# Optimization experiments

Hardware: AMD Instinct MI355X
Metric: run time of the kernel (lower is better)

Reference implementation:

```python
import jax, jax.numpy as jnp
import numpy as np

RATIO = 1.25   # res_s / res_r (1.0mm slices on 0.8mm volume grid)
N_ITER = 10


def _psf_offsets(psf):
    # psf [Kz,Ky,Kx]; offsets returned in (x,y,z) order, volume-voxel units,
    # centered integer grid (applied in the slice frame before rotation).
    Kz, Ky, Kx = psf.shape
    zs = jnp.arange(Kz, dtype=psf.dtype) - (Kz - 1) / 2.0
    ys = jnp.arange(Ky, dtype=psf.dtype) - (Ky - 1) / 2.0
    xs = jnp.arange(Kx, dtype=psf.dtype) - (Kx - 1) / 2.0
    gz, gy, gx = jnp.meshgrid(zs, ys, xs, indexing='ij')
    offs = jnp.stack([gx, gy, gz], -1).reshape(-1, 3)  # [K,3]
    return offs, psf.reshape(-1)


def _base_grid(Hs, Ws, dtype):
    # slice pixel coords, centered, scaled to volume-voxel units; (x,y,z=0)
    ys = (jnp.arange(Hs, dtype=dtype) - (Hs - 1) / 2.0) * RATIO
    xs = (jnp.arange(Ws, dtype=dtype) - (Ws - 1) / 2.0) * RATIO
    gy, gx = jnp.meshgrid(ys, xs, indexing='ij')
    return jnp.stack([gx, gy, jnp.zeros_like(gx)], -1)  # [Hs,Ws,3]


def _corners(pts, D, H, W):
    x, y, z = pts[..., 0], pts[..., 1], pts[..., 2]
    x0 = jnp.floor(x); y0 = jnp.floor(y); z0 = jnp.floor(z)
    fx, fy, fz = x - x0, y - y0, z - z0
    return (x0.astype(jnp.int32), y0.astype(jnp.int32), z0.astype(jnp.int32), fx, fy, fz)


def _trilerp_gather(vol, pts):
    # vol [D,H,W]; pts [...,3] in (x,y,z) volume-voxel coords; zero outside.
    D, H, W = vol.shape
    x0, y0, z0, fx, fy, fz = _corners(pts, D, H, W)
    out = jnp.zeros(pts.shape[:-1], vol.dtype)
    for dz in (0, 1):
        zi = z0 + dz; wz = fz if dz else (1.0 - fz); vz = (zi >= 0) & (zi < D)
        for dy in (0, 1):
            yi = y0 + dy; wy = fy if dy else (1.0 - fy); vy = vz & (yi >= 0) & (yi < H)
            for dx in (0, 1):
                xi = x0 + dx; wx = fx if dx else (1.0 - fx)
                valid = vy & (xi >= 0) & (xi < W)
                v = vol[jnp.clip(zi, 0, D - 1), jnp.clip(yi, 0, H - 1), jnp.clip(xi, 0, W - 1)]
                out = out + jnp.where(valid, wz * wy * wx * v, 0.0)
    return out


def _splat_add(vol, pts, vals):
    # adjoint of _trilerp_gather: scatter-add vals into vol at pts
    D, H, W = vol.shape
    x0, y0, z0, fx, fy, fz = _corners(pts, D, H, W)
    for dz in (0, 1):
        zi = z0 + dz; wz = fz if dz else (1.0 - fz); vz = (zi >= 0) & (zi < D)
        for dy in (0, 1):
            yi = y0 + dy; wy = fy if dy else (1.0 - fy); vy = vz & (yi >= 0) & (yi < H)
            for dx in (0, 1):
                xi = x0 + dx; wx = fx if dx else (1.0 - fx)
                valid = vy & (xi >= 0) & (xi < W)
                contrib = jnp.where(valid, wz * wy * wx * vals, 0.0)
                vol = vol.at[jnp.clip(zi, 0, D - 1), jnp.clip(yi, 0, H - 1), jnp.clip(xi, 0, W - 1)].add(contrib)
    return vol


def _points(base, off, R, t, center):
    pts = base + off                                             # [Hs,Ws,3] slice frame
    return jnp.einsum('nij,hwj->nhwi', R, pts) + t[:, None, None, :] + center  # [N,Hs,Ws,3]


def A_op(vol, transforms, psf, slice_shape):
    # slice acquisition: PSF-blurred trilinear sampling of vol along each slice
    D, H, W = vol.shape
    R, t = transforms[:, :, :3], transforms[:, :, 3]
    center = jnp.array([(W - 1) / 2.0, (H - 1) / 2.0, (D - 1) / 2.0], vol.dtype)
    base = _base_grid(slice_shape[0], slice_shape[1], vol.dtype)
    offs, w = _psf_offsets(psf)
    N = transforms.shape[0]

    def step(acc, ow):
        off, wk = ow
        ptv = _points(base, off, R, t, center)
        return acc + wk * _trilerp_gather(vol, ptv), None

    out, _ = jax.lax.scan(step, jnp.zeros((N,) + tuple(slice_shape), vol.dtype), (offs, w))
    return out


def At_op(slices, transforms, psf, vol_shape):
    # adjoint: splat PSF-weighted slice values back into the volume
    D, H, W = vol_shape
    R, t = transforms[:, :, :3], transforms[:, :, 3]
    center = jnp.array([(W - 1) / 2.0, (H - 1) / 2.0, (D - 1) / 2.0], slices.dtype)
    base = _base_grid(slices.shape[1], slices.shape[2], slices.dtype)
    offs, w = _psf_offsets(psf)

    def step(acc, ow):
        off, wk = ow
        ptv = _points(base, off, R, t, center)
        return _splat_add(acc, ptv, wk * slices), None

    out, _ = jax.lax.scan(step, jnp.zeros(vol_shape, slices.dtype), (offs, w))
    return out


def _srr_cg(vol, slices, transforms, psf):
    v = vol[0, 0]            # [D,H,W]
    y = slices[:, 0]         # [N,Hs,Ws]
    vol_shape = v.shape
    slice_shape = y.shape[1:]
    AtA = lambda x: At_op(A_op(x, transforms, psf, slice_shape), transforms, psf, vol_shape)
    b = At_op(y, transforms, psf, vol_shape)
    # CG with x0 = volume image (average_init=False), tol=0, mu=0, p=z=None
    x = v
    r = b - AtA(x)
    p = r
    rr = jnp.vdot(r, r)
    for i in range(N_ITER):
        Ap = AtA(p)
        alpha = rr / jnp.vdot(p, Ap)
        x = x + alpha * p
        if i == N_ITER - 1:
            break
        r = r - alpha * Ap
        rr_new = jnp.vdot(r, r)
        p = r + (rr_new / rr) * p
        rr = rr_new
    return jax.nn.relu(x)    # output_relu=True


def setup_inputs() -> dict:
    key = jax.random.key(0)
    k1, k2 = jax.random.split(key)
    D = H = W = 128
    N, Hs, Ws = 48, 128, 128
    vol = jax.random.uniform(k1, (1, 1, D, H, W), jnp.float32)
    slices = jax.random.uniform(k2, (N, 1, Hs, Ws), jnp.float32)
    # rigid slice->volume transforms: small random rotations, slices stacked along z
    rng = np.random.default_rng(0)
    trans = np.zeros((N, 3, 4), np.float32)
    spacing = 2.0 / 0.8  # thickness / res_r = 2.5 voxels
    for n in range(N):
        ax, ay, az = rng.uniform(-0.15, 0.15, 3)
        Rx = np.array([[1, 0, 0], [0, np.cos(ax), -np.sin(ax)], [0, np.sin(ax), np.cos(ax)]])
        Ry = np.array([[np.cos(ay), 0, np.sin(ay)], [0, 1, 0], [-np.sin(ay), 0, np.cos(ay)]])
        Rz = np.array([[np.cos(az), -np.sin(az), 0], [np.sin(az), np.cos(az), 0], [0, 0, 1]])
        trans[n, :, :3] = Rz @ Ry @ Rx
        trans[n, :, 3] = rng.uniform(-3.0, 3.0, 3)
        trans[n, 2, 3] += (n - (N - 1) / 2.0) * spacing
    # Gaussian PSF from resolution ratios: sigma_xy = 1.2*RATIO/2.3548, sigma_z = 2.5/2.3548
    def gauss(k, s):
        r = np.arange(k) - (k - 1) / 2.0
        return np.exp(-0.5 * (r / s) ** 2)
    psf = gauss(5, 2.5 / 2.3548)[:, None, None] * gauss(3, 1.2 * RATIO / 2.3548)[None, :, None] \
          * gauss(3, 1.2 * RATIO / 2.3548)[None, None, :]
    psf = (psf / psf.sum()).astype(np.float32)
    return {"vol": vol, "slices": slices, "transforms": jnp.asarray(trans), "psf": jnp.asarray(psf)}


def reference(vol, slices, transforms, psf):
    return _srr_cg(vol, slices, transforms, psf)
```

## Files before the change

kernel.cpp:

```cpp
#include <hip/hip_runtime.h>

#define NVOX (128*128*128)
#define NK 45
#define NSL 48
#define LDSF 9800

__device__ __forceinline__ float trilerp_gather_g(const float* __restrict__ v,
                                                  float x, float y, float z)
{
    float x0f = floorf(x), y0f = floorf(y), z0f = floorf(z);
    int x0 = (int)x0f, y0 = (int)y0f, z0 = (int)z0f;
    float fx = x - x0f, fy = y - y0f, fz = z - z0f;

    if (((unsigned)x0 < 127u) & ((unsigned)y0 < 127u) & ((unsigned)z0 < 127u)) {
        const float* p = v + z0*16384 + y0*128 + x0;
        float v000 = p[0],     v001 = p[1];
        float v010 = p[128],   v011 = p[129];
        float v100 = p[16384], v101 = p[16385];
        float v110 = p[16512], v111 = p[16513];
        float c00 = v000 + fx*(v001 - v000);
        float c01 = v010 + fx*(v011 - v010);
        float c10 = v100 + fx*(v101 - v100);
        float c11 = v110 + fx*(v111 - v110);
        float c0  = c00 + fy*(c01 - c00);
        float c1  = c10 + fy*(c11 - c10);
        return c0 + fz*(c1 - c0);
    }
    if (x0 < -1 || x0 > 127 || y0 < -1 || y0 > 127 || z0 < -1 || z0 > 127)
        return 0.f;
    float acc = 0.f;
#pragma unroll
    for (int dz = 0; dz < 2; ++dz) {
        int zi = z0 + dz;
        if ((unsigned)zi >= 128u) continue;
        float wz = dz ? fz : 1.f - fz;
#pragma unroll
        for (int dy = 0; dy < 2; ++dy) {
            int yi = y0 + dy;
            if ((unsigned)yi >= 128u) continue;
            float wy = dy ? fy : 1.f - fy;
#pragma unroll
            for (int dx = 0; dx < 2; ++dx) {
                int xi = x0 + dx;
                if ((unsigned)xi >= 128u) continue;
                float wx = dx ? fx : 1.f - fx;
                acc += wz*wy*wx * v[zi*16384 + yi*128 + xi];
            }
        }
    }
    return acc;
}

__device__ __forceinline__ void trilerp_splat_g(float* __restrict__ v,
                                                float x, float y, float z, float val)
{
    float x0f = floorf(x), y0f = floorf(y), z0f = floorf(z);
    int x0 = (int)x0f, y0 = (int)y0f, z0 = (int)z0f;
    float fx = x - x0f, fy = y - y0f, fz = z - z0f;
    if (x0 < -1 || x0 > 127 || y0 < -1 || y0 > 127 || z0 < -1 || z0 > 127)
        return;
#pragma unroll
    for (int dz = 0; dz < 2; ++dz) {
        int zi = z0 + dz;
        if ((unsigned)zi >= 128u) continue;
        float wz = dz ? fz : 1.f - fz;
#pragma unroll
        for (int dy = 0; dy < 2; ++dy) {
            int yi = y0 + dy;
            if ((unsigned)yi >= 128u) continue;
            float wy = dy ? fy : 1.f - fy;
#pragma unroll
            for (int dx = 0; dx < 2; ++dx) {
                int xi = x0 + dx;
                if ((unsigned)xi >= 128u) continue;
                float wx = dx ? fx : 1.f - fx;
                unsafeAtomicAdd(v + zi*16384 + yi*128 + xi, val*wz*wy*wx);
            }
        }
    }
}

__global__ void k_shifts(const float* __restrict__ trans, float* __restrict__ shifts)
{
    int i = blockIdx.x * blockDim.x + threadIdx.x;
    if (i >= NSL * NK) return;
    int n = i / NK, k = i % NK;
    int kz = k / 9, ky = (k % 9) / 3, kx = k % 3;
    float ox = (float)(kx - 1);
    float oy = (float)(ky - 1);
    float oz = (float)(kz - 2);
    const float* T = trans + n * 12;
    shifts[i*3+0] = T[0]*ox + T[1]*oy + T[2]*oz  + T[3]  + 63.5f;
    shifts[i*3+1] = T[4]*ox + T[5]*oy + T[6]*oz  + T[7]  + 63.5f;
    shifts[i*3+2] = T[8]*ox + T[9]*oy + T[10]*oz + T[11] + 63.5f;
}

__device__ __forceinline__ void block_reduce_add(double s, double* out)
{
    for (int o = 32; o > 0; o >>= 1) s += __shfl_down(s, o);
    __shared__ double ls[4];
    int lane = threadIdx.x & 63, wid = threadIdx.x >> 6;
    if (lane == 0) ls[wid] = s;
    __syncthreads();
    if (threadIdx.x == 0) atomicAdd(out, ls[0] + ls[1] + ls[2] + ls[3]);
}

__global__ __launch_bounds__(256) void k_gather(const float* __restrict__ vol,
                                                const float* __restrict__ shifts,
                                                const float* __restrict__ psf,
                                                const float* __restrict__ trans,
                                                float* __restrict__ val,
                                                float4* __restrict__ ap_zero,
                                                double* __restrict__ pap)
{
    __shared__ float sh[NK*4];
    int bid = blockIdx.x;
    int swz = (bid & 7) * (NSL * 64 / 8) + (bid >> 3);
    int n = swz >> 6, seg = swz & 63, tid = threadIdx.x;

    int zi = bid * 256 + tid;
    if (zi < NVOX/4) ap_zero[zi] = make_float4(0.f, 0.f, 0.f, 0.f);

    for (int i = tid; i < NK*3; i += 256) sh[i] = shifts[n*NK*3 + i];
    if (tid < NK) sh[NK*3+tid] = psf[tid];
    const float* T = trans + n*12;
    float R00=T[0],R01=T[1],R10=T[4],R11=T[5],R20=T[8],R21=T[9];
    __syncthreads();

    int idx = seg*256 + tid;
    int h = idx >> 7, w = idx & 127;
    float bx = ((float)w - 63.5f)*1.25f;
    float by = ((float)h - 63.5f)*1.25f;
    float rbx = R00*bx + R01*by;
    float rby = R10*bx + R11*by;
    float rbz = R20*bx + R21*by;

    float s = 0.f;
#pragma unroll 3
    for (int k = 0; k < NK; ++k)
        s += sh[NK*3+k] * trilerp_gather_g(vol, rbx + sh[k*3], rby + sh[k*3+1],
                                           rbz + sh[k*3+2]);
    val[n*16384 + idx] = s;

    block_reduce_add((double)s * (double)s, pap);
}

__global__ __launch_bounds__(64) void k_splat(const float* __restrict__ val,
                                              float* __restrict__ pout,
                                              const float* __restrict__ shifts,
                                              const float* __restrict__ psf,
                                              const float* __restrict__ trans)
{
    __shared__ float tile[LDSF];
    __shared__ float sh[NK*4];
    int n = blockIdx.x >> 6, t2 = blockIdx.x & 63;
    int th = t2 >> 3, tw = t2 & 7;
    int lane = threadIdx.x;
    int kbeg = blockIdx.y ? 27 : 0;
    int kend = blockIdx.y ? NK : 27;
    int kcnt = kend - kbeg;

    for (int i = lane; i < NK*3; i += 64) sh[i] = shifts[n*NK*3 + i];
    if (lane < NK) sh[NK*3+lane] = psf[lane];
    const float* T = trans + n*12;
    float R00=T[0],R01=T[1],R10=T[4],R11=T[5],R20=T[8],R21=T[9];
    __syncthreads();

    int kl = kbeg + ((lane < kcnt) ? lane : 0);
    float sx0 = sh[kl*3], sy0 = sh[kl*3+1], sz0 = sh[kl*3+2];
    float sxmn=sx0,sxmx=sx0,symn=sy0,symx=sy0,szmn=sz0,szmx=sz0;
    for (int o = 32; o; o >>= 1) {
        sxmn = fminf(sxmn, __shfl_xor(sxmn,o)); sxmx = fmaxf(sxmx, __shfl_xor(sxmx,o));
        symn = fminf(symn, __shfl_xor(symn,o)); symx = fmaxf(symx, __shfl_xor(symx,o));
        szmn = fminf(szmn, __shfl_xor(szmn,o)); szmx = fmaxf(szmx, __shfl_xor(szmx,o));
    }
    float cbx = ((float)(tw*16) + 7.5f - 63.5f)*1.25f;
    float cby = ((float)(th*16) + 7.5f - 63.5f)*1.25f;
    const float hs = 9.375f;
    float cx = R00*cbx + R01*cby, hx = (fabsf(R00)+fabsf(R01))*hs;
    float cy = R10*cbx + R11*cby, hy = (fabsf(R10)+fabsf(R11))*hs;
    float cz = R20*cbx + R21*cby, hz = (fabsf(R20)+fabsf(R21))*hs;
    int x_lo = (int)floorf(cx-hx+sxmn), x_hi = (int)floorf(cx+hx+sxmx)+1;
    int y_lo = (int)floorf(cy-hy+symn), y_hi = (int)floorf(cy+hy+symx)+1;
    int z_lo = (int)floorf(cz-hz+szmn), z_hi = (int)floorf(cz+hz+szmx)+1;
    int dxs  = x_hi - x_lo + 1;
    dxs |= 1;
    int dys  = y_hi - y_lo + 1;
    int dzs  = z_hi - z_lo + 1;
    int dxdy = dxs * dys;
    int total = dxdy * dzs;

    bool safe = (2.5f*(R00 - fabsf(R01)) >= 2.0f) &&
                (2.5f*(R11 - fabsf(R10)) >= 2.0f);

    if (total <= LDSF) {
        for (int c = lane; c < total; c += 64) tile[c] = 0.f;
        __syncthreads();

        float prbx[4], prby[4], prbz[4], pval[4];
#pragma unroll
        for (int p = 0; p < 4; ++p) {
            int w = tw*16 + 2*(lane & 7)  + (p & 1);
            int h = th*16 + 2*(lane >> 3) + (p >> 1);
            float bx = ((float)w - 63.5f)*1.25f;
            float by = ((float)h - 63.5f)*1.25f;
            prbx[p] = R00*bx + R01*by;
            prby[p] = R10*bx + R11*by;
            prbz[p] = R20*bx + R21*by;
            pval[p] = val[n*16384 + (h<<7) + w];
        }

#pragma unroll 1
        for (int k = kbeg; k < kend; ++k) {
            float sx = sh[k*3], sy = sh[k*3+1], sz = sh[k*3+2], wk = sh[NK*3+k];
#pragma unroll
            for (int p = 0; p < 4; ++p) {
                float x = prbx[p] + sx, y = prby[p] + sy, z = prbz[p] + sz;
                float x0f = floorf(x), y0f = floorf(y), z0f = floorf(z);
                int lx = (int)x0f - x_lo, ly = (int)y0f - y_lo, lz = (int)z0f - z_lo;
                float fx = x - x0f, fy = y - y0f, fz = z - z0f;
                float vw = pval[p] * wk;
                float wx1 = fx, wx0 = 1.f - fx;
                float wy1 = fy, wy0 = 1.f - fy;
                float wz1 = fz, wz0 = 1.f - fz;
                float* q = tile + lz*dxdy + ly*dxs + lx;
                if (safe) {
                    q[0]          += vw*wz0*wy0*wx0;
                    q[1]          += vw*wz0*wy0*wx1;
                    q[dxs]        += vw*wz0*wy1*wx0;
                    q[dxs+1]      += vw*wz0*wy1*wx1;
                    q[dxdy]       += vw*wz1*wy0*wx0;
                    q[dxdy+1]     += vw*wz1*wy0*wx1;
                    q[dxdy+dxs]   += vw*wz1*wy1*wx0;
                    q[dxdy+dxs+1] += vw*wz1*wy1*wx1;
                } else {
                    atomicAdd(q,            vw*wz0*wy0*wx0);
                    atomicAdd(q+1,          vw*wz0*wy0*wx1);
                    atomicAdd(q+dxs,        vw*wz0*wy1*wx0);
                    atomicAdd(q+dxs+1,      vw*wz0*wy1*wx1);
                    atomicAdd(q+dxdy,       vw*wz1*wy0*wx0);
                    atomicAdd(q+dxdy+1,     vw*wz1*wy0*wx1);
                    atomicAdd(q+dxdy+dxs,   vw*wz1*wy1*wx0);
                    atomicAdd(q+dxdy+dxs+1, vw*wz1*wy1*wx1);
                }
            }
        }
        __syncthreads();

        for (int c = lane; c < total; c += 64) {
            float v2 = tile[c];
            if (v2 != 0.f) {
                int lz = c / dxdy;
                int rem = c - lz*dxdy;
                int ly = rem / dxs;
                int lx = rem - ly*dxs;
                int gx = x_lo+lx, gy = y_lo+ly, gz = z_lo+lz;
                if (((unsigned)gx < 128u) & ((unsigned)gy < 128u) & ((unsigned)gz < 128u))
                    unsafeAtomicAdd(pout + gz*16384 + gy*128 + gx, v2);
            }
        }
    } else {
        for (int s2 = 0; s2 < 4; ++s2) {
            int px = s2*64 + lane;
            int ty = px >> 4, tx = px & 15;
            int h = th*16 + ty, w = tw*16 + tx;
            float bx = ((float)w - 63.5f)*1.25f;
            float by = ((float)h - 63.5f)*1.25f;
            float rbx = R00*bx + R01*by;
            float rby = R10*bx + R11*by;
            float rbz = R20*bx + R21*by;
            float v = val[n*16384 + (h<<7) + w];
#pragma unroll 1
            for (int k = kbeg; k < kend; ++k)
                trilerp_splat_g(pout, rbx + sh[k*3], rby + sh[k*3+1],
                                rbz + sh[k*3+2], sh[NK*3+k] * v);
        }
    }
}

__global__ __launch_bounds__(256) void k_init(const float* __restrict__ b,
                                              const float* __restrict__ Ax,
                                              float* __restrict__ r,
                                              float* __restrict__ p,
                                              double* rr0)
{
    double s = 0.0;
    for (int i = blockIdx.x * blockDim.x + threadIdx.x; i < NVOX;
         i += gridDim.x * blockDim.x) {
        float rv = b[i] - Ax[i];
        r[i] = rv;
        p[i] = rv;
        s += (double)rv * (double)rv;
    }
    block_reduce_add(s, rr0);
}

__global__ __launch_bounds__(256) void k_update_xr(float* __restrict__ x,
                                                   float* __restrict__ r,
                                                   const float* __restrict__ p,
                                                   const float* __restrict__ Ap,
                                                   const double* rr, const double* pap,
                                                   double* rrn, int do_r)
{
    float alpha = (float)(rr[0] / pap[0]);
    double s = 0.0;
    for (int i = blockIdx.x * blockDim.x + threadIdx.x; i < NVOX;
         i += gridDim.x * blockDim.x) {
        x[i] += alpha * p[i];
        if (do_r) {
            float rn = r[i] - alpha * Ap[i];
            r[i] = rn;
            s += (double)rn * (double)rn;
        }
    }
    block_reduce_add(s, rrn);
}

__global__ __launch_bounds__(256) void k_update_p(float* __restrict__ p,
                                                  const float* __restrict__ r,
                                                  const double* rrn, const double* rro)
{
    float beta = (float)(rrn[0] / rro[0]);
    for (int i = blockIdx.x * blockDim.x + threadIdx.x; i < NVOX;
         i += gridDim.x * blockDim.x)
        p[i] = r[i] + beta * p[i];
}

__global__ __launch_bounds__(256) void k_relu(const float* __restrict__ x,
                                              float* __restrict__ out)
{
    for (int i = blockIdx.x * blockDim.x + threadIdx.x; i < NVOX;
         i += gridDim.x * blockDim.x)
        out[i] = fmaxf(x[i], 0.f);
}

extern "C" void kernel_launch(void* const* d_in, const int* in_sizes, int n_in,
                              void* d_out, int out_size, void* d_ws, size_t ws_size,
                              hipStream_t stream)
{
    const float* vol    = (const float*)d_in[0];
    const float* slices = (const float*)d_in[1];
    const float* trans  = (const float*)d_in[2];
    const float* psf    = (const float*)d_in[3];
    float* out = (float*)d_out;

    const size_t VB = (size_t)NVOX * 4;
    char* w = (char*)d_ws;
    float* x      = (float*)(w);
    float* b      = (float*)(w + VB);
    float* r      = (float*)(w + VB*2);
    float* p      = (float*)(w + VB*3);
    float* Ap     = (float*)(w + VB*4);
    float* shifts = (float*)(w + VB*5);
    double* sc    = (double*)(w + VB*5 + 32768);
    float* val    = (float*)(w + VB*6);

    hipMemsetAsync(sc, 0, 22 * sizeof(double), stream);
    hipLaunchKernelGGL(k_shifts, dim3(9), dim3(256), 0, stream, trans, shifts);

    hipMemsetAsync(b, 0, VB, stream);
    hipLaunchKernelGGL(k_splat, dim3(NSL * 64, 2), dim3(64), 0, stream,
                       slices, b, shifts, psf, trans);

    hipMemcpyAsync(x, vol, VB, hipMemcpyDeviceToDevice, stream);

    hipLaunchKernelGGL(k_gather, dim3(NSL * 64), dim3(256), 0, stream,
                       x, shifts, psf, trans, val, (float4*)Ap, sc + 21);
    hipLaunchKernelGGL(k_splat, dim3(NSL * 64, 2), dim3(64), 0, stream,
                       val, Ap, shifts, psf, trans);

    hipLaunchKernelGGL(k_init, dim3(512), dim3(256), 0, stream, b, Ap, r, p, sc + 0);

    for (int i = 0; i < 10; ++i) {
        hipLaunchKernelGGL(k_gather, dim3(NSL * 64), dim3(256), 0, stream,
                           p, shifts, psf, trans, val, (float4*)Ap, sc + 11 + i);
        hipLaunchKernelGGL(k_splat, dim3(NSL * 64, 2), dim3(64), 0, stream,
                           val, Ap, shifts, psf, trans);
        hipLaunchKernelGGL(k_update_xr, dim3(512), dim3(256), 0, stream,
                           x, r, p, Ap, sc + i, sc + 11 + i, sc + i + 1, (int)(i < 9));
        if (i < 9)
            hipLaunchKernelGGL(k_update_p, dim3(512), dim3(256), 0, stream,
                               p, r, sc + i + 1, sc + i);
    }

    hipLaunchKernelGGL(k_relu, dim3(512), dim3(256), 0, stream, x, out);
}
```

Measured before the change: 4.712 ms.

## Split splat PSF taps into five groups with fixed-size compile-time LDS tile

The splat kernel now splits the 45 PSF taps across five blocks of nine taps (one z-plane each) instead of two uneven groups. This gives a smaller z-extent per block, so the LDS tile can be a fixed 27x27x9 box with compile-time strides, which removes the integer divides and variable indexing in the flush loop. The non-atomic LDS update is rewritten as explicit load-then-store. In exchange there are 2.5x more blocks, more redundant setup and global atomic flushes per voxel, and blocks whose footprint exceeds the fixed box fall back to the slower path.

```diff
diff --git a/kernel.cpp b/kernel.cpp
--- a/kernel.cpp
+++ b/kernel.cpp
@@ -3,7 +3,11 @@
 #define NVOX (128*128*128)
 #define NK 45
 #define NSL 48
-#define LDSF 9800
+#define DXS 27
+#define DYS 27
+#define DZS 9
+#define DXDY (DXS*DYS)
+#define SLAB (DXDY*DZS)
 
 __device__ __forceinline__ float trilerp_gather_g(const float* __restrict__ v,
                                                   float x, float y, float z)
@@ -151,14 +155,13 @@
                                               const float* __restrict__ psf,
                                               const float* __restrict__ trans)
 {
-    __shared__ float tile[LDSF];
+    __shared__ float tile[SLAB];
     __shared__ float sh[NK*4];
     int n = blockIdx.x >> 6, t2 = blockIdx.x & 63;
     int th = t2 >> 3, tw = t2 & 7;
     int lane = threadIdx.x;
-    int kbeg = blockIdx.y ? 27 : 0;
-    int kend = blockIdx.y ? NK : 27;
-    int kcnt = kend - kbeg;
+    int kbeg = blockIdx.y * 9;
+    int kend = kbeg + 9;
 
     for (int i = lane; i < NK*3; i += 64) sh[i] = shifts[n*NK*3 + i];
     if (lane < NK) sh[NK*3+lane] = psf[lane];
@@ -166,7 +169,7 @@
     float R00=T[0],R01=T[1],R10=T[4],R11=T[5],R20=T[8],R21=T[9];
     __syncthreads();
 
-    int kl = kbeg + ((lane < kcnt) ? lane : 0);
+    int kl = kbeg + ((lane < 9) ? lane : 0);
     float sx0 = sh[kl*3], sy0 = sh[kl*3+1], sz0 = sh[kl*3+2];
     float sxmn=sx0,sxmx=sx0,symn=sy0,symx=sy0,szmn=sz0,szmx=sz0;
     for (int o = 32; o; o >>= 1) {
@@ -183,18 +186,15 @@
     int x_lo = (int)floorf(cx-hx+sxmn), x_hi = (int)floorf(cx+hx+sxmx)+1;
     int y_lo = (int)floorf(cy-hy+symn), y_hi = (int)floorf(cy+hy+symx)+1;
     int z_lo = (int)floorf(cz-hz+szmn), z_hi = (int)floorf(cz+hz+szmx)+1;
-    int dxs  = x_hi - x_lo + 1;
-    dxs |= 1;
-    int dys  = y_hi - y_lo + 1;
-    int dzs  = z_hi - z_lo + 1;
-    int dxdy = dxs * dys;
-    int total = dxdy * dzs;
+    int adx = x_hi - x_lo + 1;
+    int ady = y_hi - y_lo + 1;
+    int adz = z_hi - z_lo + 1;
 
     bool safe = (2.5f*(R00 - fabsf(R01)) >= 2.0f) &&
                 (2.5f*(R11 - fabsf(R10)) >= 2.0f);
 
-    if (total <= LDSF) {
-        for (int c = lane; c < total; c += 64) tile[c] = 0.f;
+    if (adx <= DXS && ady <= DYS && adz <= DZS) {
+        for (int c = lane; c < SLAB; c += 64) tile[c] = 0.f;
         __syncthreads();
 
         float prbx[4], prby[4], prbz[4], pval[4];
@@ -223,37 +223,42 @@
                 float wx1 = fx, wx0 = 1.f - fx;
                 float wy1 = fy, wy0 = 1.f - fy;
                 float wz1 = fz, wz0 = 1.f - fz;
-                float* q = tile + lz*dxdy + ly*dxs + lx;
+                float* q  = tile + lz*DXDY + ly*DXS + lx;
+                float* q2 = q + DXDY;
                 if (safe) {
-                    q[0]          += vw*wz0*wy0*wx0;
-                    q[1]          += vw*wz0*wy0*wx1;
-                    q[dxs]        += vw*wz0*wy1*wx0;
-                    q[dxs+1]      += vw*wz0*wy1*wx1;
-                    q[dxdy]       += vw*wz1*wy0*wx0;
-                    q[dxdy+1]     += vw*wz1*wy0*wx1;
-                    q[dxdy+dxs]   += vw*wz1*wy1*wx0;
-                    q[dxdy+dxs+1] += vw*wz1*wy1*wx1;
+                    float t0 = q[0],      t1 = q[1];
+                    float t2 = q[DXS],    t3 = q[DXS+1];
+                    float t4 = q2[0],     t5 = q2[1];
+                    float t6 = q2[DXS],   t7 = q2[DXS+1];
+                    q[0]      = t0 + vw*wz0*wy0*wx0;
+                    q[1]      = t1 + vw*wz0*wy0*wx1;
+                    q[DXS]    = t2 + vw*wz0*wy1*wx0;
+                    q[DXS+1]  = t3 + vw*wz0*wy1*wx1;
+                    q2[0]     = t4 + vw*wz1*wy0*wx0;
+                    q2[1]     = t5 + vw*wz1*wy0*wx1;
+                    q2[DXS]   = t6 + vw*wz1*wy1*wx0;
+                    q2[DXS+1] = t7 + vw*wz1*wy1*wx1;
                 } else {
-                    atomicAdd(q,            vw*wz0*wy0*wx0);
-                    atomicAdd(q+1,          vw*wz0*wy0*wx1);
-                    atomicAdd(q+dxs,        vw*wz0*wy1*wx0);
-                    atomicAdd(q+dxs+1,      vw*wz0*wy1*wx1);
-                    atomicAdd(q+dxdy,       vw*wz1*wy0*wx0);
-                    atomicAdd(q+dxdy+1,     vw*wz1*wy0*wx1);
-                    atomicAdd(q+dxdy+dxs,   vw*wz1*wy1*wx0);
-                    atomicAdd(q+dxdy+dxs+1, vw*wz1*wy1*wx1);
+                    atomicAdd(q,          vw*wz0*wy0*wx0);
+                    atomicAdd(q+1,        vw*wz0*wy0*wx1);
+                    atomicAdd(q+DXS,      vw*wz0*wy1*wx0);
+                    atomicAdd(q+DXS+1,    vw*wz0*wy1*wx1);
+                    atomicAdd(q2,         vw*wz1*wy0*wx0);
+                    atomicAdd(q2+1,       vw*wz1*wy0*wx1);
+                    atomicAdd(q2+DXS,     vw*wz1*wy1*wx0);
+                    atomicAdd(q2+DXS+1,   vw*wz1*wy1*wx1);
                 }
             }
         }
         __syncthreads();
 
-        for (int c = lane; c < total; c += 64) {
+        for (int c = lane; c < SLAB; c += 64) {
             float v2 = tile[c];
             if (v2 != 0.f) {
-                int lz = c / dxdy;
-                int rem = c - lz*dxdy;
-                int ly = rem / dxs;
-                int lx = rem - ly*dxs;
+                int lz = c / DXDY;
+                int rem = c - lz*DXDY;
+                int ly = rem / DXS;
+                int lx = rem - ly*DXS;
                 int gx = x_lo+lx, gy = y_lo+ly, gz = z_lo+lz;
                 if (((unsigned)gx < 128u) & ((unsigned)gy < 128u) & ((unsigned)gz < 128u))
                     unsafeAtomicAdd(pout + gz*16384 + gy*128 + gx, v2);
@@ -359,14 +364,14 @@
     hipLaunchKernelGGL(k_shifts, dim3(9), dim3(256), 0, stream, trans, shifts);
 
     hipMemsetAsync(b, 0, VB, stream);
-    hipLaunchKernelGGL(k_splat, dim3(NSL * 64, 2), dim3(64), 0, stream,
+    hipLaunchKernelGGL(k_splat, dim3(NSL * 64, 5), dim3(64), 0, stream,
                        slices, b, shifts, psf, trans);
 
     hipMemcpyAsync(x, vol, VB, hipMemcpyDeviceToDevice, stream);
 
     hipLaunchKernelGGL(k_gather, dim3(NSL * 64), dim3(256), 0, stream,
                        x, shifts, psf, trans, val, (float4*)Ap, sc + 21);
-    hipLaunchKernelGGL(k_splat, dim3(NSL * 64, 2), dim3(64), 0, stream,
+    hipLaunchKernelGGL(k_splat, dim3(NSL * 64, 5), dim3(64), 0, stream,
                        val, Ap, shifts, psf, trans);
 
     hipLaunchKernelGGL(k_init, dim3(512), dim3(256), 0, stream, b, Ap, r, p, sc + 0);
@@ -374,7 +379,7 @@
     for (int i = 0; i < 10; ++i) {
         hipLaunchKernelGGL(k_gather, dim3(NSL * 64), dim3(256), 0, stream,
                            p, shifts, psf, trans, val, (float4*)Ap, sc + 11 + i);
-        hipLaunchKernelGGL(k_splat, dim3(NSL * 64, 2), dim3(64), 0, stream,
+        hipLaunchKernelGGL(k_splat, dim3(NSL * 64, 5), dim3(64), 0, stream,
                            val, Ap, shifts, psf, trans);
         hipLaunchKernelGGL(k_update_xr, dim3(512), dim3(256), 0, stream,
                            x, r, p, Ap, sc + i, sc + 11 + i, sc + i + 1, (int)(i < 9));
```

Result: slower. 5.000 ms (+6.1%).
